# Kernel tuning notes

Hardware: AMD Instinct MI355X
Metric: run time of the kernel (lower is better)

Reference implementation:

```python
import jax, jax.numpy as jnp
import numpy as np

N_NODES = 20000
N_EDGES = 320000
EMB = 128


def setup_inputs() -> dict:
    key = jax.random.key(0)
    ks = jax.random.split(key, 8)
    h = jax.random.normal(ks[0], (N_NODES, EMB), dtype=jnp.float32)
    W1 = jax.random.normal(ks[1], (2 * EMB, 4 * EMB), dtype=jnp.float32) / np.sqrt(2 * EMB)
    b1 = jnp.zeros((4 * EMB,), dtype=jnp.float32)
    W2 = jax.random.normal(ks[2], (4 * EMB, 1), dtype=jnp.float32) / np.sqrt(4 * EMB)
    b2 = jnp.zeros((1,), dtype=jnp.float32)
    # logistic-noise uniforms for RelaxedBernoulli rsample, kept away from {0,1}
    u = jax.random.uniform(ks[3], (N_EDGES,), dtype=jnp.float32, minval=1e-6, maxval=1.0 - 1e-6)
    row = jax.random.randint(ks[4], (N_EDGES,), 0, N_NODES, dtype=jnp.int32)
    col = jax.random.randint(ks[5], (N_EDGES,), 0, N_NODES, dtype=jnp.int32)
    edge_mask = -jnp.ones((N_EDGES,), dtype=jnp.int32)  # torch code initializes mask to -1
    return {"h": h, "W1": W1, "b1": b1, "W2": W2, "b2": b2,
            "u": u, "row": row, "col": col, "edge_mask": edge_mask, "hierarchy": 0}


def _segment_softmax(scores, seg, num_segments):
    m = jax.ops.segment_max(scores, seg, num_segments=num_segments)
    e = jnp.exp(scores - m[seg])
    s = jax.ops.segment_sum(e, seg, num_segments=num_segments)
    return e / s[seg]


TEMPERATURE = 1.0
RATIO = 0.5  # threshold for hard bernoulli


def reference(h, W1, b1, W2, b2, u, row, col, edge_mask, hierarchy):
    # edge gather + concat: [E, 2*EMB]
    edge_rep = jnp.concatenate([h[row], h[col]], axis=-1)
    # 2-layer MLP edge scorer -> [E]
    hid = jax.nn.relu(edge_rep @ W1 + b1)
    scores = (hid @ W2 + b2).reshape(-1)
    # segment softmax over edges grouped by source node (torch: softmax(edge_score, edge_index[0]))
    probs = _segment_softmax(scores, row, N_NODES)
    # RelaxedBernoulli(temperature, probs).rsample(): sigmoid((logits + logistic)/T)
    logits = jnp.log(probs) - jnp.log1p(-probs)
    logistic = jnp.log(u) - jnp.log1p(-u)
    y = jax.nn.sigmoid((logits + logistic) / TEMPERATURE)
    y_hard = (y > RATIO).astype(y.dtype)
    y_st = jax.lax.stop_gradient(y_hard - y) + y  # straight-through
    # edge_mask[y == 1] = hierarchy + 1
    new_mask = jnp.where(y_st == 1.0, jnp.int32(hierarchy + 1), edge_mask)
    c_idx = new_mask > 0
    s_idx = new_mask == -1
    causal_w = jnp.where(c_idx, scores, 0.0)
    spu_w = jnp.where(s_idx, -scores, 0.0)
    return scores, y_st, new_mask, causal_w, spu_w
```

## Files before the change

### kernel.cpp

```cpp
#include <hip/hip_runtime.h>
#include <math.h>

#define N_NODES 20000
#define N_EDGES 320000
#define EMB 128
#define HID 512
#define NCHUNK ((N_NODES + 1023) / 1024)

#define RPW 4
#define WPB 2
#define RPB (RPW * WPB)
#define FE_BLOCKS ((N_NODES + RPB - 1) / RPB)

#define GEMM_MT ((N_NODES + 255) / 256)
#define GEMM_NT 16
#define GEMM_MFMA_BLOCKS (GEMM_MT * GEMM_NT)
#define HIST_BLOCKS ((N_EDGES + 255) / 256)
#define GH_BLOCKS (GEMM_MFMA_BLOCKS + HIST_BLOCKS)
#define N_HTILES (N_NODES / 16)

#define PREP_H_BLOCKS 2500
#define PREP_W_BLOCKS 64
#define PREP_Z_BLOCKS ((N_NODES + 255) / 256)
#define PREP_BLOCKS (PREP_H_BLOCKS + PREP_W_BLOCKS + PREP_Z_BLOCKS)

typedef __attribute__((ext_vector_type(8))) short bf16x8;
typedef __attribute__((ext_vector_type(4))) float f32x4;

#define MFMA16(a, b, c) __builtin_amdgcn_mfma_f32_16x16x32_bf16((a), (b), (c), 0, 0, 0)

__device__ __forceinline__ void stage16(const unsigned short* g, unsigned short* l) {
    __builtin_amdgcn_global_load_lds(
        (const __attribute__((address_space(1))) void*)g,
        (__attribute__((address_space(3))) void*)l, 16, 0, 0);
}

__device__ __forceinline__ unsigned short bf16rn(float x) {
    unsigned u = __builtin_bit_cast(unsigned, x);
    u += 0x7FFFu + ((u >> 16) & 1u);
    return (unsigned short)(u >> 16);
}
__device__ __forceinline__ float bf2f(unsigned short b) {
    unsigned u = ((unsigned)b) << 16;
    return __builtin_bit_cast(float, u);
}
__device__ __forceinline__ void split3(float x, unsigned short& s1,
                                       unsigned short& s2, unsigned short& s3) {
    s1 = bf16rn(x);
    float r = x - bf2f(s1);
    s2 = bf16rn(r);
    float r2 = r - bf2f(s2);
    s3 = bf16rn(r2);
}

__global__ __launch_bounds__(256) void prep_pack(
    const float* __restrict__ h, const float* __restrict__ W1,
    unsigned short* __restrict__ hp1, unsigned short* __restrict__ hp2,
    unsigned short* __restrict__ hp3,
    unsigned short* __restrict__ wp1, unsigned short* __restrict__ wp2,
    unsigned short* __restrict__ wp3,
    int* __restrict__ deg, int* __restrict__ offs)
{
    const int bid = blockIdx.x, tid = threadIdx.x;

    if (bid < PREP_H_BLOCKS) {
        const int i4 = bid * 256 + tid;
        const float4 v = ((const float4*)h)[i4];
        const int r  = i4 >> 5;
        const int k0 = (i4 & 31) << 2;
        const int t = r >> 4, rowi = r & 15;
        const int ks = k0 >> 5;
        const int ln = (((k0 >> 3) & 3) << 4) + rowi;
        const int j0 = k0 & 7;
        const size_t off = (size_t)((t * 4 + ks) * 512) + ln * 8 + j0;
        unsigned short a1[4], a2[4], a3[4];
        split3(v.x, a1[0], a2[0], a3[0]);
        split3(v.y, a1[1], a2[1], a3[1]);
        split3(v.z, a1[2], a2[2], a3[2]);
        split3(v.w, a1[3], a2[3], a3[3]);
#define PACK4(dst, a) { \
            uint2 pk; \
            pk.x = (unsigned)a[0] | ((unsigned)a[1] << 16); \
            pk.y = (unsigned)a[2] | ((unsigned)a[3] << 16); \
            *(uint2*)((dst) + off) = pk; }
        PACK4(hp1, a1); PACK4(hp2, a2); PACK4(hp3, a3);
#undef PACK4
        return;
    }

    if (bid < PREP_H_BLOCKS + PREP_W_BLOCKS) {
        const int t = (bid - PREP_H_BLOCKS) * 256 + tid;
        const int n = t & 1023, kg = t >> 10;
        const int k0 = kg << 3;
        const int wrow0 = ((n >> 9) << 7) + k0;
        const int wcol  = n & 511;
        unsigned short s1[8], s2[8], s3[8];
#pragma unroll
        for (int j = 0; j < 8; ++j) {
            const float x = W1[(size_t)(wrow0 + j) * HID + wcol];
            split3(x, s1[j], s2[j], s3[j]);
        }
        const int tn = n >> 4, rown = n & 15;
        const int ks = k0 >> 5;
        const int ln = (((k0 >> 3) & 3) << 4) + rown;
        const size_t off = (size_t)((tn * 4 + ks) * 512) + ln * 8;
#define PACK8(dst, a) { \
            uint4 pk; \
            pk.x = (unsigned)a[0] | ((unsigned)a[1] << 16); \
            pk.y = (unsigned)a[2] | ((unsigned)a[3] << 16); \
            pk.z = (unsigned)a[4] | ((unsigned)a[5] << 16); \
            pk.w = (unsigned)a[6] | ((unsigned)a[7] << 16); \
            *(uint4*)((dst) + off) = pk; }
        PACK8(wp1, s1); PACK8(wp2, s2); PACK8(wp3, s3);
#undef PACK8
        return;
    }

    const int i = (bid - PREP_H_BLOCKS - PREP_W_BLOCKS) * 256 + tid;
    if (i < N_NODES) deg[i] = 0;
    if (i == 0) offs[N_NODES] = N_EDGES;
}

__global__ __launch_bounds__(256, 2) void gemm_mfma(
    const unsigned short* __restrict__ hp1, const unsigned short* __restrict__ hp2,
    const unsigned short* __restrict__ hp3,
    const unsigned short* __restrict__ wp1, const unsigned short* __restrict__ wp2,
    const unsigned short* __restrict__ wp3,
    const float* __restrict__ b1, float* __restrict__ P, float* __restrict__ Q,
    const int* __restrict__ row, int* __restrict__ deg)
{
    const int bid = blockIdx.x;
    const int tid = threadIdx.x;

    if (bid >= GEMM_MFMA_BLOCKS) {
        const int e = (bid - GEMM_MFMA_BLOCKS) * 256 + tid;
        if (e < N_EDGES) atomicAdd(&deg[row[e]], 1);
        return;
    }

    __shared__ unsigned short bs[4][4][3][512];

    const int mt = bid >> 4, nt = bid & 15;
    const int lane = tid & 63, w = tid >> 6;
    const int l15 = lane & 15, l4 = lane >> 4;

    {
        const int tn = nt * 4 + w;
        const unsigned short* wps0 = wp1;
        const unsigned short* wps1 = wp2;
        const unsigned short* wps2 = wp3;
#pragma unroll
        for (int ks = 0; ks < 4; ++ks) {
            const size_t so = (size_t)((tn * 4 + ks) * 512) + lane * 8;
            stage16(wps0 + so, &bs[w][ks][0][0]);
            stage16(wps1 + so, &bs[w][ks][1][0]);
            stage16(wps2 + so, &bs[w][ks][2][0]);
        }
    }

    int tA[4];
#pragma unroll
    for (int i = 0; i < 4; ++i) {
        int t = mt * 16 + w * 4 + i;
        tA[i] = (t < N_HTILES) ? t : N_HTILES - 1;
    }
    size_t aoff[4];
#pragma unroll
    for (int i = 0; i < 4; ++i)
        aoff[i] = (size_t)(tA[i] * 4) * 512 + lane * 8;

    bf16x8 A1[4], A2[4], A3[4];
#pragma unroll
    for (int i = 0; i < 4; ++i) {
        A1[i] = *(const bf16x8*)(hp1 + aoff[i]);
        A2[i] = *(const bf16x8*)(hp2 + aoff[i]);
        A3[i] = *(const bf16x8*)(hp3 + aoff[i]);
    }

    f32x4 acc[4][4];
#pragma unroll
    for (int i = 0; i < 4; ++i)
#pragma unroll
        for (int j = 0; j < 4; ++j) acc[i][j] = (f32x4){0.f, 0.f, 0.f, 0.f};

    __syncthreads();

#pragma unroll
    for (int ks = 0; ks < 4; ++ks) {
        bf16x8 N1[4], N2[4], N3[4];
        if (ks < 3) {
            const size_t ko = (size_t)(ks + 1) * 512;
#pragma unroll
            for (int i = 0; i < 4; ++i) {
                N1[i] = *(const bf16x8*)(hp1 + aoff[i] + ko);
                N2[i] = *(const bf16x8*)(hp2 + aoff[i] + ko);
                N3[i] = *(const bf16x8*)(hp3 + aoff[i] + ko);
            }
        }
#pragma unroll
        for (int jn = 0; jn < 4; ++jn) {
            const unsigned short* bb = &bs[jn][ks][0][0] + lane * 8;
            const bf16x8 Ba1 = *(const bf16x8*)(bb);
            const bf16x8 Ba2 = *(const bf16x8*)(bb + 512);
            const bf16x8 Ba3 = *(const bf16x8*)(bb + 1024);
#pragma unroll
            for (int i = 0; i < 4; ++i) {
                acc[i][jn] = MFMA16(A1[i], Ba1, acc[i][jn]);
                acc[i][jn] = MFMA16(A1[i], Ba2, acc[i][jn]);
                acc[i][jn] = MFMA16(A2[i], Ba1, acc[i][jn]);
                acc[i][jn] = MFMA16(A2[i], Ba2, acc[i][jn]);
                acc[i][jn] = MFMA16(A1[i], Ba3, acc[i][jn]);
                acc[i][jn] = MFMA16(A3[i], Ba1, acc[i][jn]);
            }
        }
        if (ks < 3) {
#pragma unroll
            for (int i = 0; i < 4; ++i) {
                A1[i] = N1[i]; A2[i] = N2[i]; A3[i] = N3[i];
            }
        }
    }

    const int rb0 = mt * 256 + w * 64;
#pragma unroll
    for (int jn = 0; jn < 4; ++jn) {
        const int n = nt * 64 + jn * 16 + l15;
        const bool isP = n < 512;
        float* __restrict__ dst = isP ? P : Q;
        const int col = n & 511;
        const float bias = isP ? b1[col] : 0.0f;
#pragma unroll
        for (int i = 0; i < 4; ++i) {
            const int rr0 = rb0 + i * 16 + l4 * 4;
#pragma unroll
            for (int r = 0; r < 4; ++r) {
                const int rr = rr0 + r;
                if (rr < N_NODES)
                    dst[(size_t)rr * HID + col] = acc[i][jn][r] + bias;
            }
        }
    }
}

__device__ __forceinline__ int wave_incl_scan(int v, int lane) {
#pragma unroll
    for (int off = 1; off < 64; off <<= 1) {
        int t = __shfl_up(v, off, 64);
        if (lane >= off) v += t;
    }
    return v;
}

__global__ __launch_bounds__(1024) void scan_part(const int* __restrict__ deg,
                                                  int* __restrict__ part,
                                                  int* __restrict__ totals) {
    __shared__ int wsum[16];
    const int tid = threadIdx.x, lane = tid & 63, w = tid >> 6;
    const int i = blockIdx.x * 1024 + tid;
    int v = (i < N_NODES) ? deg[i] : 0;
    int incl = wave_incl_scan(v, lane);
    if (lane == 63) wsum[w] = incl;
    __syncthreads();
    if (w == 0) {
        int x = (lane < 16) ? wsum[lane] : 0;
        int xs = wave_incl_scan(x, lane);
        if (lane < 16) wsum[lane] = xs - x;
        if (lane == 15) totals[blockIdx.x] = xs;
    }
    __syncthreads();
    if (i < N_NODES) part[i] = wsum[w] + incl - v;
}

__global__ __launch_bounds__(1024) void scan_apply(const int* __restrict__ part,
                                                   const int* __restrict__ totals,
                                                   int* __restrict__ cursor,
                                                   int* __restrict__ offs) {
    __shared__ int carry_s;
    const int tid = threadIdx.x;
    if (tid < 64) {
        int v = (tid < NCHUNK) ? totals[tid] : 0;
        int incl = wave_incl_scan(v, tid);
        if (tid == (int)blockIdx.x) carry_s = incl - v;
    }
    __syncthreads();
    const int i = blockIdx.x * 1024 + tid;
    if (i < N_NODES) {
        int o = part[i] + carry_s;
        cursor[i] = o;
        offs[i] = o;
    }
}

__global__ void scatter_edges(const int* __restrict__ row, const int* __restrict__ col,
                              int* __restrict__ cursor,
                              unsigned short* __restrict__ cols16,
                              int* __restrict__ inv) {
    int e = blockIdx.x * 256 + threadIdx.x;
    if (e >= N_EDGES) return;
    int r = row[e];
    int pos = atomicAdd(&cursor[r], 1);
    cols16[pos] = (unsigned short)col[e];
    inv[e] = pos;
}

__device__ __forceinline__ float dot8_relu(const float4 qa, const float4 qb,
                                           const float4 p0, const float4 p1,
                                           const float4 w0, const float4 w1) {
    float t = 0.0f;
    t = fmaf(fmaxf(p0.x + qa.x, 0.0f), w0.x, t);
    t = fmaf(fmaxf(p0.y + qa.y, 0.0f), w0.y, t);
    t = fmaf(fmaxf(p0.z + qa.z, 0.0f), w0.z, t);
    t = fmaf(fmaxf(p0.w + qa.w, 0.0f), w0.w, t);
    t = fmaf(fmaxf(p1.x + qb.x, 0.0f), w1.x, t);
    t = fmaf(fmaxf(p1.y + qb.y, 0.0f), w1.y, t);
    t = fmaf(fmaxf(p1.z + qb.z, 0.0f), w1.z, t);
    t = fmaf(fmaxf(p1.w + qb.w, 0.0f), w1.w, t);
    return t;
}

__device__ __forceinline__ float chunk_scores(
    const float* __restrict__ Q, const unsigned short* __restrict__ cols16,
    int es_base, int nch, int lane, int j0,
    const float4 p0, const float4 p1, const float4 w0, const float4 w1,
    float bias2)
{
    int mycol = 0;
    if (lane < nch) mycol = (int)cols16[es_base + lane];
    float mysc = -INFINITY;

#define QL2(k, bb, d0, d1) { \
        int c_ = __shfl(mycol, (bb) + (k), 64); \
        const float* __restrict__ q_ = Q + (size_t)c_ * HID; \
        d0 = *(const float4*)(q_ + j0); \
        d1 = *(const float4*)(q_ + 256 + j0); }

    float4 a00, a01, a10, a11;
    QL2(0, 0, a00, a01); QL2(1, 0, a10, a11);

    for (int b = 0; b < nch; b += 2) {
        float4 n00, n01, n10, n11;
        const bool more = (b + 2) < nch;
        if (more) { QL2(0, b + 2, n00, n01); QL2(1, b + 2, n10, n11); }

        float s0 = dot8_relu(a00, a01, p0, p1, w0, w1);
        float s1 = dot8_relu(a10, a11, p0, p1, w0, w1);

#pragma unroll
        for (int off = 32; off > 0; off >>= 1) {
            s0 += __shfl_xor(s0, off, 64);
            s1 += __shfl_xor(s1, off, 64);
        }

        const int k = lane - b;
        if ((unsigned)k < 2u && lane < nch) mysc = (k ? s1 : s0) + bias2;

        if (more) { a00 = n00; a01 = n01; a10 = n10; a11 = n11; }
    }
#undef QL2
    return mysc;
}

__global__ __launch_bounds__(128) void fused_edge(
    const float* __restrict__ P, const float* __restrict__ Q,
    const float* __restrict__ W2, const float* __restrict__ b2,
    const unsigned short* __restrict__ cols16, const int* __restrict__ offs,
    float2* __restrict__ tmp)
{
    const int tid = threadIdx.x, lane = tid & 63, w = tid >> 6;
    const int r0 = blockIdx.x * RPB + w * RPW;
    const int r1 = (r0 + RPW < N_NODES) ? r0 + RPW : N_NODES;
    const int j0 = lane << 2;

    const float4 w0 = *(const float4*)(W2 + j0);
    const float4 w1 = *(const float4*)(W2 + 256 + j0);
    const float bias2 = b2[0];

    for (int r = r0; r < r1; ++r) {
        const int es = offs[r], ee = offs[r + 1];
        const int d = ee - es;
        if (d == 0) continue;

        const float* __restrict__ prow = P + (size_t)r * HID;
        const float4 p0 = *(const float4*)(prow + j0);
        const float4 p1 = *(const float4*)(prow + 256 + j0);

        if (d <= 64) {
            float mysc = chunk_scores(Q, cols16, es, d, lane, j0,
                                      p0, p1, w0, w1, bias2);

            float m = mysc;
#pragma unroll
            for (int off = 32; off > 0; off >>= 1)
                m = fmaxf(m, __shfl_xor(m, off, 64));

            float ev = (lane < d) ? expf(mysc - m) : 0.0f;
            float ssum = ev;
#pragma unroll
            for (int off = 32; off > 0; off >>= 1)
                ssum += __shfl_xor(ssum, off, 64);

            if (lane < d) {
                float p = ev / ssum;
                float logits = logf(p) - log1pf(-p);
                tmp[es + lane] = make_float2(mysc, logits);
            }
        } else {
            for (int base = 0; base < d; base += 64) {
                const int nch = (d - base < 64) ? d - base : 64;
                float mysc = chunk_scores(Q, cols16, es + base, nch, lane, j0,
                                          p0, p1, w0, w1, bias2);
                if (lane < nch) tmp[es + base + lane].x = mysc;
            }

            float m = -INFINITY;
            for (int j = lane; j < d; j += 64)
                m = fmaxf(m, tmp[es + j].x);
#pragma unroll
            for (int off = 32; off > 0; off >>= 1)
                m = fmaxf(m, __shfl_xor(m, off, 64));

            float ssum = 0.0f;
            for (int j = lane; j < d; j += 64)
                ssum += expf(tmp[es + j].x - m);
#pragma unroll
            for (int off = 32; off > 0; off >>= 1)
                ssum += __shfl_xor(ssum, off, 64);

            for (int j = lane; j < d; j += 64) {
                float s = tmp[es + j].x;
                float p = expf(s - m) / ssum;
                float logits = logf(p) - log1pf(-p);
                tmp[es + j] = make_float2(s, logits);
            }
        }
    }
}

__global__ __launch_bounds__(256) void unperm(
    const float2* __restrict__ tmp, const int* __restrict__ inv,
    const float* __restrict__ u, const int* __restrict__ edge_mask,
    const int* __restrict__ hierarchy,
    float* __restrict__ scores, float* __restrict__ out_y,
    float* __restrict__ out_mask, float* __restrict__ out_causal,
    float* __restrict__ out_spu)
{
    const int e = blockIdx.x * 256 + threadIdx.x;
    if (e >= N_EDGES) return;
    const float2 t = tmp[inv[e]];
    const float s = t.x;
    const float uu = u[e];
    const float L = logf(uu) - log1pf(-uu);
    const float y = 1.0f / (1.0f + expf(-(t.y + L)));
    const bool hard = y > 0.5f;
    const int mm = hard ? (hierarchy[0] + 1) : edge_mask[e];
    scores[e]     = s;
    out_y[e]      = hard ? 1.0f : 0.0f;
    out_mask[e]   = (float)mm;
    out_causal[e] = (mm > 0)   ?  s : 0.0f;
    out_spu[e]    = (mm == -1) ? -s : 0.0f;
}

extern "C" void kernel_launch(void* const* d_in, const int* in_sizes, int n_in,
                              void* d_out, int out_size, void* d_ws, size_t ws_size,
                              hipStream_t stream) {
    const float* h_ptr = (const float*)d_in[0];
    const float* W1    = (const float*)d_in[1];
    const float* b1    = (const float*)d_in[2];
    const float* W2    = (const float*)d_in[3];
    const float* b2    = (const float*)d_in[4];
    const float* u     = (const float*)d_in[5];
    const int*   row   = (const int*)d_in[6];
    const int*   col   = (const int*)d_in[7];
    const int*   emask = (const int*)d_in[8];
    const int*   hier  = (const int*)d_in[9];

    float* out        = (float*)d_out;
    float* scores     = out;
    float* out_y      = out + (size_t)N_EDGES;
    float* out_mask   = out + 2 * (size_t)N_EDGES;
    float* out_causal = out + 3 * (size_t)N_EDGES;
    float* out_spu    = out + 4 * (size_t)N_EDGES;

    float*          P      = (float*)d_ws;
    float*          Qm     = P + (size_t)N_NODES * HID;
    unsigned short* hp1    = (unsigned short*)(Qm + (size_t)N_NODES * HID);
    unsigned short* hp2    = hp1 + (size_t)N_NODES * EMB;
    unsigned short* hp3    = hp2 + (size_t)N_NODES * EMB;
    unsigned short* wp1    = hp3 + (size_t)N_NODES * EMB;
    unsigned short* wp2    = wp1 + 1024 * 128;
    unsigned short* wp3    = wp2 + 1024 * 128;
    int*            deg    = (int*)(wp3 + 1024 * 128);
    int*            cursor = deg + N_NODES;
    int*            offs   = cursor + N_NODES;
    int*            part   = offs + N_NODES + 1;
    int*            totals = part + N_NODES;
    float2*         tmp    = (float2*)hp1;
    unsigned short* cols16 = (unsigned short*)(tmp + N_EDGES);
    int*            inv    = (int*)(cols16 + N_EDGES);

    hipLaunchKernelGGL(prep_pack, dim3(PREP_BLOCKS), dim3(256), 0, stream,
                       h_ptr, W1, hp1, hp2, hp3, wp1, wp2, wp3, deg, offs);

    hipLaunchKernelGGL(gemm_mfma, dim3(GH_BLOCKS), dim3(256), 0, stream,
                       hp1, hp2, hp3, wp1, wp2, wp3, b1, P, Qm, row, deg);

    hipLaunchKernelGGL(scan_part, dim3(NCHUNK), dim3(1024), 0, stream, deg, part, totals);
    hipLaunchKernelGGL(scan_apply, dim3(NCHUNK), dim3(1024), 0, stream,
                       part, totals, cursor, offs);
    hipLaunchKernelGGL(scatter_edges, dim3((N_EDGES + 255) / 256), dim3(256), 0, stream,
                       row, col, cursor, cols16, inv);

    hipLaunchKernelGGL(fused_edge, dim3(FE_BLOCKS), dim3(128), 0, stream,
                       P, Qm, W2, b2, cols16, offs, tmp);

    hipLaunchKernelGGL(unperm, dim3((N_EDGES + 255) / 256), dim3(256), 0, stream,
                       tmp, inv, u, emask, hier,
                       scores, out_y, out_mask, out_causal, out_spu);
}
```

Baseline: 262.3 us.

## Swizzle GEMM block order, reorder MFMA loop, resize edge-kernel blocks

Remaps GEMM block IDs with an 8-way interleave so that consecutively dispatched blocks are spread across tiles, likely to spread work across XCDs or improve cache locality. Reorders the MFMA inner loop so that each B fragment is read from shared memory once per split pass instead of three fragments together, which lowers register pressure but issues more LDS reads in sequence. Changes the fused_edge kernel to 4 waves of 2 rows each (256 threads) instead of 2 waves of 4 rows, so each wave handles fewer rows, balancing load better across degree variation.

Result: faster. 253.7 us (-3.3%).

```diff
diff --git a/kernel.cpp b/kernel.cpp
--- a/kernel.cpp
+++ b/kernel.cpp
@@ -7,8 +7,8 @@
 #define HID 512
 #define NCHUNK ((N_NODES + 1023) / 1024)
 
-#define RPW 4
-#define WPB 2
+#define RPW 2
+#define WPB 4
 #define RPB (RPW * WPB)
 #define FE_BLOCKS ((N_NODES + RPB - 1) / RPB)
 
@@ -140,21 +140,19 @@
 
     __shared__ unsigned short bs[4][4][3][512];
 
-    const int mt = bid >> 4, nt = bid & 15;
+    const int lb = (bid & 7) * (GEMM_MFMA_BLOCKS / 8) + (bid >> 3);
+    const int mt = lb >> 4, nt = lb & 15;
     const int lane = tid & 63, w = tid >> 6;
     const int l15 = lane & 15, l4 = lane >> 4;
 
     {
         const int tn = nt * 4 + w;
-        const unsigned short* wps0 = wp1;
-        const unsigned short* wps1 = wp2;
-        const unsigned short* wps2 = wp3;
 #pragma unroll
         for (int ks = 0; ks < 4; ++ks) {
             const size_t so = (size_t)((tn * 4 + ks) * 512) + lane * 8;
-            stage16(wps0 + so, &bs[w][ks][0][0]);
-            stage16(wps1 + so, &bs[w][ks][1][0]);
-            stage16(wps2 + so, &bs[w][ks][2][0]);
+            stage16(wp1 + so, &bs[w][ks][0][0]);
+            stage16(wp2 + so, &bs[w][ks][1][0]);
+            stage16(wp3 + so, &bs[w][ks][2][0]);
         }
     }
 
@@ -197,22 +195,16 @@
                 N3[i] = *(const bf16x8*)(hp3 + aoff[i] + ko);
             }
         }
-#pragma unroll
-        for (int jn = 0; jn < 4; ++jn) {
-            const unsigned short* bb = &bs[jn][ks][0][0] + lane * 8;
-            const bf16x8 Ba1 = *(const bf16x8*)(bb);
-            const bf16x8 Ba2 = *(const bf16x8*)(bb + 512);
-            const bf16x8 Ba3 = *(const bf16x8*)(bb + 1024);
-#pragma unroll
-            for (int i = 0; i < 4; ++i) {
-                acc[i][jn] = MFMA16(A1[i], Ba1, acc[i][jn]);
-                acc[i][jn] = MFMA16(A1[i], Ba2, acc[i][jn]);
-                acc[i][jn] = MFMA16(A2[i], Ba1, acc[i][jn]);
-                acc[i][jn] = MFMA16(A2[i], Ba2, acc[i][jn]);
-                acc[i][jn] = MFMA16(A1[i], Ba3, acc[i][jn]);
-                acc[i][jn] = MFMA16(A3[i], Ba1, acc[i][jn]);
-            }
-        }
+#define PROD(AA, SP) \
+        { _Pragma("unroll") \
+          for (int jn = 0; jn < 4; ++jn) { \
+              const bf16x8 Bv = *(const bf16x8*)(&bs[jn][ks][SP][0] + lane * 8); \
+              _Pragma("unroll") \
+              for (int i = 0; i < 4; ++i) \
+                  acc[i][jn] = MFMA16(AA[i], Bv, acc[i][jn]); \
+          } }
+        PROD(A1, 0) PROD(A1, 1) PROD(A2, 0) PROD(A2, 1) PROD(A1, 2) PROD(A3, 0)
+#undef PROD
         if (ks < 3) {
 #pragma unroll
             for (int i = 0; i < 4; ++i) {
@@ -360,7 +352,7 @@
     return mysc;
 }
 
-__global__ __launch_bounds__(128) void fused_edge(
+__global__ __launch_bounds__(256) void fused_edge(
     const float* __restrict__ P, const float* __restrict__ Q,
     const float* __restrict__ W2, const float* __restrict__ b2,
     const unsigned short* __restrict__ cols16, const int* __restrict__ offs,
@@ -510,7 +502,7 @@
     hipLaunchKernelGGL(scatter_edges, dim3((N_EDGES + 255) / 256), dim3(256), 0, stream,
                        row, col, cursor, cols16, inv);
 
-    hipLaunchKernelGGL(fused_edge, dim3(FE_BLOCKS), dim3(128), 0, stream,
+    hipLaunchKernelGGL(fused_edge, dim3(FE_BLOCKS), dim3(256), 0, stream,
                        P, Qm, W2, b2, cols16, offs, tmp);
 
     hipLaunchKernelGGL(unperm, dim3((N_EDGES + 255) / 256), dim3(256), 0, stream,
```
